# Kernel tuning notes

Hardware: AMD Instinct MI355X
Metric: run time of the kernel (lower is better)

## Reference

```python
import jax, jax.numpy as jnp
import numpy as np


def setup_inputs() -> dict:
    key = jax.random.key(0)
    k1, k2 = jax.random.split(key)
    N, D, T = 1_000_000, 128, 1_000_000
    triplets = jax.random.randint(k1, (T, 3), 0, N, dtype=jnp.int64)
    node_emb = jax.random.normal(k2, (N, D), dtype=jnp.float32)
    vars = jnp.zeros((1,), dtype=jnp.float32)  # unused by forward (parity with original signature)
    return {"triplets": triplets, "node_emb": node_emb, "vars": vars}


def reference(triplets, node_emb, vars) -> jnp.ndarray:
    # gather left/right node embeddings, per-triplet dot product -> [T]
    left = node_emb[triplets[:, 0]]   # [T, D]
    right = node_emb[triplets[:, 2]]  # [T, D]
    scores = jnp.einsum('td,td->t', left, right)
    return scores
```

## Files before the change

kernel.cpp:

```cpp
#include <hip/hip_runtime.h>
#include <hip/hip_bf16.h>

constexpr int U = 8;

__global__ __launch_bounds__(256) void dot_gather_kernel(
    const int* __restrict__ trip,
    const float* __restrict__ emb,
    float* __restrict__ out,
    int T) {
  int gid = blockIdx.x * blockDim.x + threadIdx.x;
  int group = gid >> 5;
  int lane = gid & 31;
  long long t0 = (long long)group * U;
  if (t0 >= T) return;

  int iL[U], iR[U];
  #pragma unroll
  for (int u = 0; u < U; ++u) {
    long long t = (t0 + u < T) ? (t0 + u) : (long long)(T - 1);
    iL[u] = trip[3 * t];
    iR[u] = trip[3 * t + 2];
  }

  float4 a[U], b[U];
  #pragma unroll
  for (int u = 0; u < U; ++u) {
    a[u] = ((const float4*)(emb + (long long)iL[u] * 128))[lane];
    b[u] = ((const float4*)(emb + (long long)iR[u] * 128))[lane];
  }

  #pragma unroll
  for (int u = 0; u < U; ++u) {
    float s = a[u].x * b[u].x + a[u].y * b[u].y + a[u].z * b[u].z + a[u].w * b[u].w;
    #pragma unroll
    for (int off = 16; off > 0; off >>= 1)
      s += __shfl_down(s, off, 32);
    if (lane == 0 && t0 + u < T) out[t0 + u] = s;
  }
}

extern "C" void kernel_launch(void* const* d_in, const int* in_sizes, int n_in,
                              void* d_out, int out_size, void* d_ws, size_t ws_size,
                              hipStream_t stream) {
  const int* trip = (const int*)d_in[0];
  const float* emb = (const float*)d_in[1];
  float* out = (float*)d_out;

  int T = in_sizes[0] / 3;
  long long groups = ((long long)T + U - 1) / U;
  long long total_threads = groups * 32;
  int block = 256;
  long long grid = (total_threads + block - 1) / block;

  dot_gather_kernel<<<(int)grid, block, 0, stream>>>(trip, emb, out, T);
}
```

Measured before the change: 698.3 us.

## Use persistent grid-stride loop with prefetch of next tile's indices

Replaces the one-shot kernel with a fixed grid of 4096 blocks that loop over tiles in grid-stride order. The triplet indices for the next tile are prefetched while the current tile's embedding rows are loaded, and U drops from 8 to 4. Output writes become nontemporal stores. The aim is to hide index-load latency ahead of the dependent gathers, at the cost of fewer loads in flight per iteration.

```diff
diff --git a/kernel.cpp b/kernel.cpp
--- a/kernel.cpp
+++ b/kernel.cpp
@@ -1,41 +1,69 @@
 #include <hip/hip_runtime.h>
 #include <hip/hip_bf16.h>
 
-constexpr int U = 8;
+constexpr int U = 4;
 
 __global__ __launch_bounds__(256) void dot_gather_kernel(
     const int* __restrict__ trip,
     const float* __restrict__ emb,
     float* __restrict__ out,
-    int T) {
+    int T, int ngroups) {
   int gid = blockIdx.x * blockDim.x + threadIdx.x;
   int group = gid >> 5;
   int lane = gid & 31;
-  long long t0 = (long long)group * U;
-  if (t0 >= T) return;
+  long long ntiles = ((long long)T + U - 1) / U;
+
+  long long tile = group;
+  if (tile >= ntiles) return;
 
   int iL[U], iR[U];
-  #pragma unroll
-  for (int u = 0; u < U; ++u) {
-    long long t = (t0 + u < T) ? (t0 + u) : (long long)(T - 1);
-    iL[u] = trip[3 * t];
-    iR[u] = trip[3 * t + 2];
+  {
+    long long t0 = tile * U;
+    #pragma unroll
+    for (int u = 0; u < U; ++u) {
+      long long t = (t0 + u < T) ? (t0 + u) : (long long)(T - 1);
+      iL[u] = trip[3 * t];
+      iR[u] = trip[3 * t + 2];
+    }
   }
 
-  float4 a[U], b[U];
-  #pragma unroll
-  for (int u = 0; u < U; ++u) {
-    a[u] = ((const float4*)(emb + (long long)iL[u] * 128))[lane];
-    b[u] = ((const float4*)(emb + (long long)iR[u] * 128))[lane];
-  }
+  while (true) {
+    long long t0 = tile * U;
+    long long next = tile + ngroups;
 
-  #pragma unroll
-  for (int u = 0; u < U; ++u) {
-    float s = a[u].x * b[u].x + a[u].y * b[u].y + a[u].z * b[u].z + a[u].w * b[u].w;
+    float4 a[U], b[U];
     #pragma unroll
-    for (int off = 16; off > 0; off >>= 1)
-      s += __shfl_down(s, off, 32);
-    if (lane == 0 && t0 + u < T) out[t0 + u] = s;
+    for (int u = 0; u < U; ++u) {
+      a[u] = ((const float4*)(emb + (long long)iL[u] * 128))[lane];
+      b[u] = ((const float4*)(emb + (long long)iR[u] * 128))[lane];
+    }
+
+    int jL[U], jR[U];
+    bool have_next = (next < ntiles);
+    if (have_next) {
+      long long n0 = next * U;
+      #pragma unroll
+      for (int u = 0; u < U; ++u) {
+        long long t = (n0 + u < T) ? (n0 + u) : (long long)(T - 1);
+        jL[u] = trip[3 * t];
+        jR[u] = trip[3 * t + 2];
+      }
+    }
+
+    #pragma unroll
+    for (int u = 0; u < U; ++u) {
+      float s = a[u].x * b[u].x + a[u].y * b[u].y + a[u].z * b[u].z + a[u].w * b[u].w;
+      #pragma unroll
+      for (int off = 16; off > 0; off >>= 1)
+        s += __shfl_down(s, off, 32);
+      if (lane == 0 && t0 + u < T)
+        __builtin_nontemporal_store(s, &out[t0 + u]);
+    }
+
+    if (!have_next) break;
+    tile = next;
+    #pragma unroll
+    for (int u = 0; u < U; ++u) { iL[u] = jL[u]; iR[u] = jR[u]; }
   }
 }
 
@@ -47,10 +75,9 @@
   float* out = (float*)d_out;
 
   int T = in_sizes[0] / 3;
-  long long groups = ((long long)T + U - 1) / U;
-  long long total_threads = groups * 32;
   int block = 256;
-  long long grid = (total_threads + block - 1) / block;
+  int grid = 4096;
+  int ngroups = grid * block / 32;
 
-  dot_gather_kernel<<<(int)grid, block, 0, stream>>>(trip, emb, out, T);
+  dot_gather_kernel<<<grid, block, 0, stream>>>(trip, emb, out, T, ngroups);
 }
```

Result: no change. 711.0 us (+1.8%).
